# Kernel optimization log

Hardware: AMD Instinct MI355X
Metric: run time of the kernel (lower is better)

## Reference

```python
import jax, jax.numpy as jnp
import numpy as np

B, T, D, H, W = 4, 4096, 1024, 16, 64  # batch, seq, dim, heads, window_size
HD = D // H
NW = T // W  # num_windows (T divisible by W -> pad=0)


def setup_inputs() -> dict:
    key = jax.random.key(0)
    ks = jax.random.split(key, 7)
    x = jax.random.normal(ks[0], (B, T, D), dtype=jnp.float32)
    W_qkv = jax.random.normal(ks[1], (3 * D, D), dtype=jnp.float32) * 0.02
    W_out = jax.random.normal(ks[2], (D, D), dtype=jnp.float32) * 0.02
    b_out = jnp.zeros((D,), dtype=jnp.float32)
    W_cross = jax.random.normal(ks[3], (D, D), dtype=jnp.float32) * 0.02
    b_cross = jnp.zeros((D,), dtype=jnp.float32)
    jitter = jax.random.permutation(ks[4], NW)  # fixed permutation (stands in for torch.randperm)
    return {"x": x, "W_qkv": W_qkv, "W_out": W_out, "b_out": b_out,
            "W_cross": W_cross, "b_cross": b_cross, "jitter": jitter}


def reference(x, W_qkv, W_out, b_out, W_cross, b_cross, jitter):
    scale = HD ** -0.5
    # qkv projection (no bias)
    qkv = x @ W_qkv.T                      # (B,T,3D)
    q, k, v = jnp.split(qkv, 3, axis=-1)

    def to_windows(t):  # (B,T,D) -> (B,H,NW,W,HD)
        return t.reshape(B, T, H, HD).transpose(0, 2, 1, 3).reshape(B, H, NW, W, HD)

    q_w, k_w, v_w = to_windows(q), to_windows(k), to_windows(v)

    # local windowed attention
    attn = jnp.einsum('bhnqd,bhnkd->bhnqk', q_w, k_w) * scale
    attn = jax.nn.softmax(attn, axis=-1)
    local = jnp.einsum('bhnqk,bhnkd->bhnqd', attn, v_w)      # (B,H,NW,W,HD)
    local = local.reshape(B, H, T, HD).transpose(0, 2, 1, 3).reshape(B, T, D)

    # cross-window summary exchange
    scores = jnp.tanh(x @ W_cross.T + b_cross).mean(-1)       # (B,T)
    weights = jax.nn.softmax(scores.reshape(B, NW, W), axis=-1)
    summaries = jnp.einsum('bnw,bnwd->bnd', weights, x.reshape(B, NW, W, D))  # (B,NW,D)
    jittered = summaries[:, jitter, :]
    cs_attn = jax.nn.softmax(jnp.einsum('bnd,bmd->bnm', summaries, jittered) * (D ** -0.5), axis=-1)
    cs_out = jnp.einsum('bnm,bmd->bnd', cs_attn, jittered)    # (B,NW,D)
    cs_exp = jnp.broadcast_to(cs_out[:, :, None, :], (B, NW, W, D)).reshape(B, T, D)

    final = local + 0.25 * cs_exp
    return final @ W_out.T + b_out
```

## Files before the change

kernel.cpp:

```cpp
#include <hip/hip_runtime.h>

typedef unsigned short u16;
typedef float f32x4 __attribute__((ext_vector_type(4)));
typedef __bf16 bf16x8 __attribute__((ext_vector_type(8)));

#define T_ 4096
#define D_ 1024
#define NW_ 64

__device__ __forceinline__ float b2f(u16 u) {
  return __uint_as_float(((unsigned)u) << 16);
}
__device__ __forceinline__ u16 f2bf(float f) {
  unsigned u = __float_as_uint(f);
  u += 0x7fffu + ((u >> 16) & 1u);
  return (u16)(u >> 16);
}
__device__ __forceinline__ void g2l16(const u16* g, u16* l) {
  __builtin_amdgcn_global_load_lds((const __attribute__((address_space(1))) void*)g,
                                   (__attribute__((address_space(3))) void*)l, 16, 0, 0);
}

__global__ __launch_bounds__(256) void cvt3_k(const float* __restrict__ s0, u16* __restrict__ d0,
                                              const float* __restrict__ s1, u16* __restrict__ d1,
                                              const float* __restrict__ s2, u16* __restrict__ d2)
{
  long bid = blockIdx.x;
  const float* src; u16* dst; long base;
  if (bid < 16384)      { src = s0; dst = d0; base = bid * 1024; }
  else if (bid < 19456) { src = s1; dst = d1; base = (bid - 16384) * 1024; }
  else                  { src = s2; dst = d2; base = (bid - 19456) * 1024; }
  long i = base + (long)threadIdx.x * 4;
  float4 v = *(const float4*)(src + i);
  ushort4 o;
  o.x = f2bf(v.x); o.y = f2bf(v.y); o.z = f2bf(v.z); o.w = f2bf(v.w);
  *(ushort4*)(dst + i) = o;
}

__global__ __launch_bounds__(256) void cvt_k(const float* __restrict__ src,
                                             u16* __restrict__ dst, long n)
{
  long i = ((long)blockIdx.x * 256 + threadIdx.x) * 4;
  if (i >= n) return;
  float4 v = *(const float4*)(src + i);
  ushort4 o;
  o.x = f2bf(v.x); o.y = f2bf(v.y); o.z = f2bf(v.z); o.w = f2bf(v.w);
  *(ushort4*)(dst + i) = o;
}

__global__ __launch_bounds__(512, 2) void gemm256(
    const u16* __restrict__ A, const u16* __restrict__ Bm,
    u16* __restrict__ C16, float* __restrict__ C32,
    const float* __restrict__ bias, int M, int N, int K, int lda)
{
  __shared__ u16 SH[65536];
  (void)M;
  const int tid = threadIdx.x;
  const int lane = tid & 63;
  const int w = tid >> 6;
  const int wm = w >> 2, wn = w & 3;
  const int q = lane >> 4, il = lane & 15;

  const int nbx = gridDim.x;
  const int nwg = nbx * (int)gridDim.y;
  const int bid = (int)blockIdx.y * nbx + (int)blockIdx.x;
  const int nid = (bid & 7) * (nwg >> 3) + (bid >> 3);
  const long m0 = (long)(nid / nbx) * 256;
  const long n0 = (long)(nid % nbx) * 256;

  const int nt = K >> 6;
  const int ntm1 = nt - 1;

  const int u0 = tid, u1 = 512 + tid;
  const int r0 = u0 >> 3, r1 = u1 >> 3;
  const int sx0 = ((u0 & 7) ^ (r0 & 7)) << 3;
  const int sx1 = ((u1 & 7) ^ (r1 & 7)) << 3;
  const long gar0 = m0 + (r0 >> 6) * 128 + (r0 & 63);
  const long gar1 = m0 + (r1 >> 6) * 128 + (r1 & 63);
  const long gbr0 = n0 + (r0 >> 5) * 64 + (r0 & 31);
  const long gbr1 = n0 + (r1 >> 5) * 64 + (r1 & 31);
  const int dl = w * 512;

  const int aro = (wm * 64 + il) * 64;
  const int bro = (wn * 32 + il) * 64;
  const int ax = (il & 7) << 3;
  const int ko0 = (q * 8) ^ ax;
  const int ko1 = (32 + q * 8) ^ ax;

  f32x4 acc[8][4] = {};
  bf16x8 af[4][2], bf0[2][2], bf1[2][2];

#define ASP(BUF, MH) (&SH[((BUF) * 2 + (MH)) * 8192])
#define BSP(BUF, NH) (&SH[32768 + ((BUF) * 2 + (NH)) * 8192])
#define STGA(BUF, MH, KT) do { \
    g2l16(A + (gar0 + (MH) * 64) * (long)lda + (KT) * 64 + sx0, ASP(BUF, MH) + dl); \
    g2l16(A + (gar1 + (MH) * 64) * (long)lda + (KT) * 64 + sx1, ASP(BUF, MH) + 4096 + dl); \
  } while (0)
#define STGB(BUF, NH, KT) do { \
    g2l16(Bm + (gbr0 + (NH) * 32) * (long)K + (KT) * 64 + sx0, BSP(BUF, NH) + dl); \
    g2l16(Bm + (gbr1 + (NH) * 32) * (long)K + (KT) * 64 + sx1, BSP(BUF, NH) + 4096 + dl); \
  } while (0)
#define LDAF(BUF, MH) do { \
    _Pragma("unroll") for (int f = 0; f < 4; ++f) { \
      af[f][0] = *(const bf16x8*)(ASP(BUF, MH) + aro + f * 1024 + ko0); \
      af[f][1] = *(const bf16x8*)(ASP(BUF, MH) + aro + f * 1024 + ko1); \
    } } while (0)
#define LDBF(BUF, NH, BF) do { \
    _Pragma("unroll") for (int j = 0; j < 2; ++j) { \
      BF[j][0] = *(const bf16x8*)(BSP(BUF, NH) + bro + j * 1024 + ko0); \
      BF[j][1] = *(const bf16x8*)(BSP(BUF, NH) + bro + j * 1024 + ko1); \
    } } while (0)
#define MFMAQ(MH, NH, BF) do { \
    _Pragma("unroll") for (int f = 0; f < 4; ++f) { \
      _Pragma("unroll") for (int j = 0; j < 2; ++j) { \
        acc[(MH)*4+f][(NH)*2+j] = __builtin_amdgcn_mfma_f32_16x16x32_bf16(af[f][0], BF[j][0], acc[(MH)*4+f][(NH)*2+j], 0, 0, 0); \
        acc[(MH)*4+f][(NH)*2+j] = __builtin_amdgcn_mfma_f32_16x16x32_bf16(af[f][1], BF[j][1], acc[(MH)*4+f][(NH)*2+j], 0, 0, 0); \
      } } } while (0)
#define BARR() __builtin_amdgcn_s_barrier()
#define WL0() asm volatile("s_waitcnt lgkmcnt(0)" ::: "memory")
#define WV6() asm volatile("s_waitcnt vmcnt(6)" ::: "memory")
#define PRIO(x) __builtin_amdgcn_s_setprio(x)

  STGA(0, 0, 0); STGB(0, 0, 0); STGB(0, 1, 0); STGA(0, 1, 0);
  STGA(1, 0, 1); STGB(1, 0, 1); STGB(1, 1, 1);
  WV6();
  BARR();

  for (int tt = 0; tt < nt; tt += 2) {
    const int t1 = tt + 1;
    const int t2 = tt + 2 <= ntm1 ? tt + 2 : ntm1;
    const int t3 = tt + 3 <= ntm1 ? tt + 3 : ntm1;
    LDAF(0, 0); LDBF(0, 0, bf0);
    STGA(1, 1, t1);
    BARR(); WL0();
    PRIO(1); MFMAQ(0, 0, bf0); PRIO(0);
    BARR();
    LDBF(0, 1, bf1);
    STGA(0, 0, t2);
    BARR(); WL0();
    PRIO(1); MFMAQ(0, 1, bf1); PRIO(0);
    BARR();
    LDAF(0, 1);
    STGB(0, 0, t2);
    BARR(); WL0();
    PRIO(1); MFMAQ(1, 0, bf0); PRIO(0);
    BARR();
    STGB(0, 1, t2);
    BARR();
    PRIO(1); MFMAQ(1, 1, bf1); PRIO(0);
    WV6(); BARR();
    LDAF(1, 0); LDBF(1, 0, bf0);
    STGA(0, 1, t2);
    BARR(); WL0();
    PRIO(1); MFMAQ(0, 0, bf0); PRIO(0);
    BARR();
    LDBF(1, 1, bf1);
    STGA(1, 0, t3);
    BARR(); WL0();
    PRIO(1); MFMAQ(0, 1, bf1); PRIO(0);
    BARR();
    LDAF(1, 1);
    STGB(1, 0, t3);
    BARR(); WL0();
    PRIO(1); MFMAQ(1, 0, bf0); PRIO(0);
    BARR();
    STGB(1, 1, t3);
    BARR();
    PRIO(1); MFMAQ(1, 1, bf1); PRIO(0);
    WV6(); BARR();
  }

  asm volatile("s_waitcnt vmcnt(0)" ::: "memory");
  __syncthreads();

  if (C32) {
    float* Cf = (float*)SH;
#pragma unroll
    for (int h = 0; h < 2; ++h) {
      if (wm == h) {
#pragma unroll
        for (int ni = 0; ni < 4; ++ni) {
          const int ccol = wn * 64 + ni * 16 + il;
          const float bv = bias ? bias[n0 + ccol] : 0.0f;
#pragma unroll
          for (int mi = 0; mi < 8; ++mi) {
#pragma unroll
            for (int r = 0; r < 4; ++r) {
              const int crow = (mi >> 2) * 64 + (mi & 3) * 16 + q * 4 + r;
              const int byte = (crow * 1024 + ccol * 4) ^ (((crow >> 2) & 1) << 6);
              *(float*)((char*)Cf + byte) = acc[mi][ni][r] + bv;
            }
          }
        }
      }
      __syncthreads();
#pragma unroll
      for (int i = 0; i < 16; ++i) {
        const int u = i * 512 + tid;
        const int crow = u >> 6, c16 = u & 63;
        const int byte = (crow * 1024 + c16 * 16) ^ (((crow >> 2) & 1) << 6);
        float4 v = *(const float4*)((char*)Cf + byte);
        *(float4*)(C32 + (m0 + h * 128 + crow) * N + n0 + c16 * 4) = v;
      }
      __syncthreads();
    }
  } else {
    u16* Cs = (u16*)SH;
#pragma unroll
    for (int ni = 0; ni < 4; ++ni) {
      const int ccol = wn * 64 + ni * 16 + il;
      const float bv = bias ? bias[n0 + ccol] : 0.0f;
#pragma unroll
      for (int mi = 0; mi < 8; ++mi) {
#pragma unroll
        for (int r = 0; r < 4; ++r) {
          const int crow = wm * 128 + (mi >> 2) * 64 + (mi & 3) * 16 + q * 4 + r;
          const int byte = (crow * 512 + ccol * 2) ^ (((crow >> 2) & 3) << 5);
          *(u16*)((char*)Cs + byte) = f2bf(acc[mi][ni][r] + bv);
        }
      }
    }
    __syncthreads();
#pragma unroll
    for (int i = 0; i < 16; ++i) {
      const int u = i * 512 + tid;
      const int crow = u >> 5, c16 = u & 31;
      const int byte = (crow * 512 + c16 * 16) ^ (((crow >> 2) & 3) << 5);
      uint4 v = *(const uint4*)((char*)Cs + byte);
      *(uint4*)(C16 + (m0 + crow) * N + n0 + c16 * 8) = v;
    }
  }
#undef ASP
#undef BSP
#undef STGA
#undef STGB
#undef LDAF
#undef LDBF
#undef MFMAQ
#undef BARR
#undef WL0
#undef WV6
#undef PRIO
}

__global__ __launch_bounds__(256) void scores_k(const u16* __restrict__ y,
                                                float* __restrict__ scores)
{
  const int lane = threadIdx.x & 63;
  const long r = (long)blockIdx.x * 4 + (threadIdx.x >> 6);
  const u16* p = y + r * D_ + lane * 16;
  uint4 v0 = *(const uint4*)p;
  uint4 v1 = *(const uint4*)(p + 8);
  union { uint4 v; u16 s[8]; } a, c;
  a.v = v0; c.v = v1;
  float s = 0.f;
#pragma unroll
  for (int e = 0; e < 8; ++e) s += tanhf(b2f(a.s[e]));
#pragma unroll
  for (int e = 0; e < 8; ++e) s += tanhf(b2f(c.s[e]));
#pragma unroll
  for (int o = 32; o; o >>= 1) s += __shfl_xor(s, o, 64);
  if (lane == 0) scores[r] = s * (1.0f / 1024.0f);
}

__global__ __launch_bounds__(256) void summar_k(const float* __restrict__ x,
                                                const float* __restrict__ scores,
                                                float* __restrict__ summ)
{
  __shared__ float wts[64];
  const int tid = threadIdx.x;
  const int b = blockIdx.x >> 6, n = blockIdx.x & 63;
  if (tid < 64) {
    float v = scores[(long)b * T_ + n * 64 + tid];
    float mx = v;
#pragma unroll
    for (int o = 32; o; o >>= 1) mx = fmaxf(mx, __shfl_xor(mx, o, 64));
    float e = __expf(v - mx);
    float s = e;
#pragma unroll
    for (int o = 32; o; o >>= 1) s += __shfl_xor(s, o, 64);
    wts[tid] = e / s;
  }
  __syncthreads();
  const int d0 = tid * 4;
  const float* xp = x + ((long)b * T_ + n * 64) * D_ + d0;
  float a0 = 0, a1 = 0, a2 = 0, a3 = 0;
#pragma unroll 4
  for (int wd = 0; wd < 64; ++wd) {
    float4 v = *(const float4*)(xp + (long)wd * D_);
    float wv = wts[wd];
    a0 += wv * v.x; a1 += wv * v.y; a2 += wv * v.z; a3 += wv * v.w;
  }
  *(float4*)(summ + ((long)b * NW_ + n) * D_ + d0) = make_float4(a0, a1, a2, a3);
}

__global__ __launch_bounds__(256) void cross_k(const float* __restrict__ summ,
                                               const int* __restrict__ jitter,
                                               float* __restrict__ cso)
{
  __shared__ float sm[64], pm[64];
  __shared__ int jidx[64];
  const int tid = threadIdx.x;
  const int b = blockIdx.x >> 6, n = blockIdx.x & 63;
  if (tid < 64) jidx[tid] = jitter[tid];
  __syncthreads();
  const int m = tid >> 2, part = tid & 3;
  const float* sn = summ + ((long)b * NW_ + n) * D_;
  const float* sj = summ + ((long)b * NW_ + jidx[m]) * D_;
  float p = 0.f;
  for (int d = part * 256; d < part * 256 + 256; d += 4) {
    float4 aa = *(const float4*)(sn + d);
    float4 bb = *(const float4*)(sj + d);
    p += aa.x * bb.x + aa.y * bb.y + aa.z * bb.z + aa.w * bb.w;
  }
  p += __shfl_xor(p, 1, 64);
  p += __shfl_xor(p, 2, 64);
  if (part == 0) sm[m] = p * (1.0f / 32.0f);
  __syncthreads();
  if (tid < 64) {
    float v = sm[tid], mx = v;
#pragma unroll
    for (int o = 32; o; o >>= 1) mx = fmaxf(mx, __shfl_xor(mx, o, 64));
    float e = __expf(v - mx), s = e;
#pragma unroll
    for (int o = 32; o; o >>= 1) s += __shfl_xor(s, o, 64);
    pm[tid] = e / s;
  }
  __syncthreads();
  const int d0 = tid * 4;
  float a0 = 0, a1 = 0, a2 = 0, a3 = 0;
  for (int mm = 0; mm < 64; ++mm) {
    const float* sr = summ + ((long)b * NW_ + jidx[mm]) * D_ + d0;
    float wv = pm[mm];
    float4 vv = *(const float4*)sr;
    a0 += wv * vv.x; a1 += wv * vv.y; a2 += wv * vv.z; a3 += wv * vv.w;
  }
  *(float4*)(cso + ((long)b * NW_ + n) * D_ + d0) = make_float4(a0, a1, a2, a3);
}

__global__ __launch_bounds__(256) void attn_win(u16* qkv,
                                                const float* __restrict__ cso)
{
  __shared__ u16 Qs[64 * 72], Ks[64 * 72], Vt[64 * 72], Ps[64 * 72];
  unsigned* Vt32 = (unsigned*)Vt;
  const int tid = threadIdx.x;
  const int lane = tid & 63;
  const int w = tid >> 6;
  const int q = lane >> 4, il = lane & 15;
  const int bid = blockIdx.x;
  const int n = bid & 63;
  const int h = (bid >> 6) & 15;
  const int b = bid >> 10;
  const long rowbase = (long)b * T_ + n * 64;

#pragma unroll
  for (int i = 0; i < 2; ++i) {
    int u = i * 256 + tid;
    int row = u >> 3, cp = u & 7;
    const u16* src = qkv + (rowbase + row) * 3072 + h * 64 + cp * 8;
    uint4 qv = *(const uint4*)src;
    uint4 kv = *(const uint4*)(src + 1024);
    uint4 vv = *(const uint4*)(src + 2048);
    *(uint4*)&Qs[row * 72 + cp * 8] = qv;
    *(uint4*)&Ks[row * 72 + cp * 8] = kv;
    union { uint4 v; unsigned u[4]; } mine, part;
    mine.v = vv;
#pragma unroll
    for (int m = 0; m < 4; ++m) part.u[m] = __shfl_xor(mine.u[m], 8, 64);
    const bool even = ((row & 1) == 0);
    const int p = row >> 1;
#pragma unroll
    for (int m = 0; m < 4; ++m) {
      unsigned word = even ? ((mine.u[m] & 0xffffu) | (part.u[m] << 16))
                           : ((part.u[m] >> 16)     | (mine.u[m] & 0xffff0000u));
      int c = cp * 8 + 2 * m + (even ? 0 : 1);
      Vt32[c * 36 + p] = word;
    }
  }
  __syncthreads();

  f32x4 sacc[4] = {};
#pragma unroll
  for (int ks = 0; ks < 2; ++ks) {
    bf16x8 aq = *(const bf16x8*)&Qs[(w * 16 + il) * 72 + ks * 32 + q * 8];
#pragma unroll
    for (int ct = 0; ct < 4; ++ct) {
      bf16x8 bk = *(const bf16x8*)&Ks[(ct * 16 + il) * 72 + ks * 32 + q * 8];
      sacc[ct] = __builtin_amdgcn_mfma_f32_16x16x32_bf16(aq, bk, sacc[ct], 0, 0, 0);
    }
  }

#pragma unroll
  for (int r = 0; r < 4; ++r) {
    float s0 = sacc[0][r] * 0.125f, s1 = sacc[1][r] * 0.125f,
          s2 = sacc[2][r] * 0.125f, s3 = sacc[3][r] * 0.125f;
    float mx = fmaxf(fmaxf(s0, s1), fmaxf(s2, s3));
#pragma unroll
    for (int o = 1; o < 16; o <<= 1) mx = fmaxf(mx, __shfl_xor(mx, o, 64));
    float e0 = __expf(s0 - mx), e1 = __expf(s1 - mx),
          e2 = __expf(s2 - mx), e3 = __expf(s3 - mx);
    float sum = e0 + e1 + e2 + e3;
#pragma unroll
    for (int o = 1; o < 16; o <<= 1) sum += __shfl_xor(sum, o, 64);
    float inv = 1.0f / sum;
    int prow = w * 16 + q * 4 + r;
    Ps[prow * 72 + 0 * 16 + il] = f2bf(e0 * inv);
    Ps[prow * 72 + 1 * 16 + il] = f2bf(e1 * inv);
    Ps[prow * 72 + 2 * 16 + il] = f2bf(e2 * inv);
    Ps[prow * 72 + 3 * 16 + il] = f2bf(e3 * inv);
  }
  __syncthreads();

  f32x4 oacc[4] = {};
#pragma unroll
  for (int ks = 0; ks < 2; ++ks) {
    bf16x8 ap = *(const bf16x8*)&Ps[(w * 16 + il) * 72 + ks * 32 + q * 8];
#pragma unroll
    for (int dt = 0; dt < 4; ++dt) {
      bf16x8 bv = *(const bf16x8*)&Vt[(dt * 16 + il) * 72 + ks * 32 + q * 8];
      oacc[dt] = __builtin_amdgcn_mfma_f32_16x16x32_bf16(ap, bv, oacc[dt], 0, 0, 0);
    }
  }

  const float* cs = cso + ((long)b * NW_ + n) * D_ + h * 64;
#pragma unroll
  for (int dt = 0; dt < 4; ++dt) {
    int col = dt * 16 + il;
    float cadd = 0.25f * cs[col];
#pragma unroll
    for (int r = 0; r < 4; ++r) {
      int row = w * 16 + q * 4 + r;
      qkv[(rowbase + row) * 3072 + h * 64 + col] = f2bf(oacc[dt][r] + cadd);
    }
  }
}

extern "C" void kernel_launch(void* const* d_in, const int* in_sizes, int n_in,
                              void* d_out, int out_size, void* d_ws, size_t ws_size,
                              hipStream_t stream)
{
  (void)in_sizes; (void)n_in; (void)out_size; (void)ws_size;
  const float* x      = (const float*)d_in[0];
  const float* Wqkv   = (const float*)d_in[1];
  const float* Wout   = (const float*)d_in[2];
  const float* bout   = (const float*)d_in[3];
  const float* Wcross = (const float*)d_in[4];
  const float* bcross = (const float*)d_in[5];
  const int*   jitter = (const int*)d_in[6];
  float* out = (float*)d_out;

  char* ws = (char*)d_ws;
  u16*   qkv    = (u16*)ws;
  u16*   y      = (u16*)ws;
  u16*   xb     = (u16*)(ws + 100663296);
  u16*   wqkvb  = (u16*)(ws + 134217728);
  u16*   wtmp   = (u16*)(ws + 140509184);
  float* scores = (float*)(ws + 142606336);
  float* summ   = (float*)(ws + 142671872);
  float* cso    = (float*)(ws + 143720448);

  dim3 blk(256);
  dim3 gblk(512);
  cvt3_k<<<20480, blk, 0, stream>>>(x, xb, Wqkv, wqkvb, Wcross, wtmp);
  gemm256<<<dim3(4, 64), gblk, 0, stream>>>(xb, wtmp, y, nullptr, bcross, 16384, 1024, 1024, 1024);
  cvt_k<<<1024, blk, 0, stream>>>(Wout, wtmp, 1048576L);
  scores_k<<<4096, blk, 0, stream>>>(y, scores);
  summar_k<<<256, blk, 0, stream>>>(x, scores, summ);
  cross_k<<<256, blk, 0, stream>>>(summ, jitter, cso);
  gemm256<<<dim3(12, 64), gblk, 0, stream>>>(xb, wqkvb, qkv, nullptr, nullptr, 16384, 3072, 1024, 1024);
  attn_win<<<4096, blk, 0, stream>>>(qkv, cso);
  gemm256<<<dim3(4, 64), gblk, 0, stream>>>(qkv, wtmp, nullptr, out, bout, 16384, 1024, 1024, 3072);
}
```

Baseline: 379.0 us.

## Software-pipeline LDS fragment loads with MFMA using double-buffered A registers

Restructures the GEMM main loop so the LDS fragment reads for the next quarter-tile are issued before the MFMA block of the current one. This uses a second A-fragment register set and drops the explicit lgkmcnt(0) waits. The global-to-LDS staging wait changes from vmcnt(6) to vmcnt(8), and one barrier per quarter is removed. The aim is to hide LDS latency and cut barrier stalls, at the cost of more VGPRs and a riskier ordering of LDS reuse against in-flight staging writes.

```diff
diff --git a/kernel.cpp b/kernel.cpp
--- a/kernel.cpp
+++ b/kernel.cpp
@@ -88,7 +88,7 @@
   const int ko1 = (32 + q * 8) ^ ax;
 
   f32x4 acc[8][4] = {};
-  bf16x8 af[4][2], bf0[2][2], bf1[2][2];
+  bf16x8 afA[4][2], afB[4][2], bf0[2][2], bf1[2][2];
 
 #define ASP(BUF, MH) (&SH[((BUF) * 2 + (MH)) * 8192])
 #define BSP(BUF, NH) (&SH[32768 + ((BUF) * 2 + (NH)) * 8192])
@@ -100,74 +100,66 @@
     g2l16(Bm + (gbr0 + (NH) * 32) * (long)K + (KT) * 64 + sx0, BSP(BUF, NH) + dl); \
     g2l16(Bm + (gbr1 + (NH) * 32) * (long)K + (KT) * 64 + sx1, BSP(BUF, NH) + 4096 + dl); \
   } while (0)
-#define LDAF(BUF, MH) do { \
+#define LDAF(BUF, MH, AF) do { \
     _Pragma("unroll") for (int f = 0; f < 4; ++f) { \
-      af[f][0] = *(const bf16x8*)(ASP(BUF, MH) + aro + f * 1024 + ko0); \
-      af[f][1] = *(const bf16x8*)(ASP(BUF, MH) + aro + f * 1024 + ko1); \
+      AF[f][0] = *(const bf16x8*)(ASP(BUF, MH) + aro + f * 1024 + ko0); \
+      AF[f][1] = *(const bf16x8*)(ASP(BUF, MH) + aro + f * 1024 + ko1); \
     } } while (0)
 #define LDBF(BUF, NH, BF) do { \
     _Pragma("unroll") for (int j = 0; j < 2; ++j) { \
       BF[j][0] = *(const bf16x8*)(BSP(BUF, NH) + bro + j * 1024 + ko0); \
       BF[j][1] = *(const bf16x8*)(BSP(BUF, NH) + bro + j * 1024 + ko1); \
     } } while (0)
-#define MFMAQ(MH, NH, BF) do { \
+#define MFMAQ(MH, NH, AF, BF) do { \
     _Pragma("unroll") for (int f = 0; f < 4; ++f) { \
       _Pragma("unroll") for (int j = 0; j < 2; ++j) { \
-        acc[(MH)*4+f][(NH)*2+j] = __builtin_amdgcn_mfma_f32_16x16x32_bf16(af[f][0], BF[j][0], acc[(MH)*4+f][(NH)*2+j], 0, 0, 0); \
-        acc[(MH)*4+f][(NH)*2+j] = __builtin_amdgcn_mfma_f32_16x16x32_bf16(af[f][1], BF[j][1], acc[(MH)*4+f][(NH)*2+j], 0, 0, 0); \
+        acc[(MH)*4+f][(NH)*2+j] = __builtin_amdgcn_mfma_f32_16x16x32_bf16(AF[f][0], BF[j][0], acc[(MH)*4+f][(NH)*2+j], 0, 0, 0); \
+        acc[(MH)*4+f][(NH)*2+j] = __builtin_amdgcn_mfma_f32_16x16x32_bf16(AF[f][1], BF[j][1], acc[(MH)*4+f][(NH)*2+j], 0, 0, 0); \
       } } } while (0)
 #define BARR() __builtin_amdgcn_s_barrier()
-#define WL0() asm volatile("s_waitcnt lgkmcnt(0)" ::: "memory")
-#define WV6() asm volatile("s_waitcnt vmcnt(6)" ::: "memory")
+#define WV8() asm volatile("s_waitcnt vmcnt(8)" ::: "memory")
 #define PRIO(x) __builtin_amdgcn_s_setprio(x)
 
   STGA(0, 0, 0); STGB(0, 0, 0); STGB(0, 1, 0); STGA(0, 1, 0);
   STGA(1, 0, 1); STGB(1, 0, 1); STGB(1, 1, 1);
-  WV6();
+  WV8();
   BARR();
+  LDAF(0, 0, afA); LDBF(0, 0, bf0);
 
   for (int tt = 0; tt < nt; tt += 2) {
     const int t1 = tt + 1;
     const int t2 = tt + 2 <= ntm1 ? tt + 2 : ntm1;
     const int t3 = tt + 3 <= ntm1 ? tt + 3 : ntm1;
-    LDAF(0, 0); LDBF(0, 0, bf0);
+    LDBF(0, 1, bf1);
+    PRIO(1); MFMAQ(0, 0, afA, bf0); PRIO(0);
     STGA(1, 1, t1);
-    BARR(); WL0();
-    PRIO(1); MFMAQ(0, 0, bf0); PRIO(0);
+    WV8(); BARR();
+    LDAF(0, 1, afB);
+    PRIO(1); MFMAQ(0, 1, afA, bf1); PRIO(0);
+    STGA(0, 0, t2);
     BARR();
-    LDBF(0, 1, bf1);
-    STGA(0, 0, t2);
-    BARR(); WL0();
-    PRIO(1); MFMAQ(0, 1, bf1); PRIO(0);
+    PRIO(1); MFMAQ(1, 0, afB, bf0); PRIO(0);
+    STGB(0, 0, t2);
+    WV8(); BARR();
+    LDAF(1, 0, afA); LDBF(1, 0, bf0);
+    PRIO(1); MFMAQ(1, 1, afB, bf1); PRIO(0);
+    STGB(0, 1, t2);
+    WV8(); BARR();
+    LDBF(1, 1, bf1);
+    PRIO(1); MFMAQ(0, 0, afA, bf0); PRIO(0);
+    STGA(0, 1, t2);
+    WV8(); BARR();
+    LDAF(1, 1, afB);
+    PRIO(1); MFMAQ(0, 1, afA, bf1); PRIO(0);
+    STGA(1, 0, t3);
     BARR();
-    LDAF(0, 1);
-    STGB(0, 0, t2);
-    BARR(); WL0();
-    PRIO(1); MFMAQ(1, 0, bf0); PRIO(0);
-    BARR();
-    STGB(0, 1, t2);
-    BARR();
-    PRIO(1); MFMAQ(1, 1, bf1); PRIO(0);
-    WV6(); BARR();
-    LDAF(1, 0); LDBF(1, 0, bf0);
-    STGA(0, 1, t2);
-    BARR(); WL0();
-    PRIO(1); MFMAQ(0, 0, bf0); PRIO(0);
-    BARR();
-    LDBF(1, 1, bf1);
-    STGA(1, 0, t3);
-    BARR(); WL0();
-    PRIO(1); MFMAQ(0, 1, bf1); PRIO(0);
-    BARR();
-    LDAF(1, 1);
+    PRIO(1); MFMAQ(1, 0, afB, bf0); PRIO(0);
     STGB(1, 0, t3);
-    BARR(); WL0();
-    PRIO(1); MFMAQ(1, 0, bf0); PRIO(0);
-    BARR();
+    WV8(); BARR();
+    LDAF(0, 0, afA); LDBF(0, 0, bf0);
+    PRIO(1); MFMAQ(1, 1, afB, bf1); PRIO(0);
     STGB(1, 1, t3);
-    BARR();
-    PRIO(1); MFMAQ(1, 1, bf1); PRIO(0);
-    WV6(); BARR();
+    WV8(); BARR();
   }
 
   asm volatile("s_waitcnt vmcnt(0)" ::: "memory");
@@ -238,8 +230,7 @@
 #undef LDBF
 #undef MFMAQ
 #undef BARR
-#undef WL0
-#undef WV6
+#undef WV8
 #undef PRIO
 }
 
```

Result: slower. 411.0 us (+8.4%).

## Fuse cross-score GEMM and tanh-mean reduction into the QKV GEMM launch

Applied to the files above, without the earlier changes.

Extends the QKV GEMM grid with four extra column blocks that multiply x by W_cross. This relies on the bf16 W_cross buffer sitting right after W_qkv in the workspace. Those blocks apply bias and tanh in registers, reduce each row across lanes and waves, and write per-tile partial scores, which summar_k sums. This drops the bf16 y intermediate write and read, the separate scores_k kernel and one GEMM launch, and gives a larger grid with better tail balance. The cost is a heavier epilogue in those blocks, reliance on the adjacent buffer layout, and reuse of d_out as scratch for the cross-summary output.

```diff
diff --git a/kernel.cpp b/kernel.cpp
--- a/kernel.cpp
+++ b/kernel.cpp
@@ -51,7 +51,8 @@
 __global__ __launch_bounds__(512, 2) void gemm256(
     const u16* __restrict__ A, const u16* __restrict__ Bm,
     u16* __restrict__ C16, float* __restrict__ C32,
-    const float* __restrict__ bias, int M, int N, int K, int lda)
+    const float* __restrict__ bias, int M, int N, int K, int lda,
+    float* __restrict__ scores4, const float* __restrict__ bias_y)
 {
   __shared__ u16 SH[65536];
   (void)M;
@@ -88,7 +89,7 @@
   const int ko1 = (32 + q * 8) ^ ax;
 
   f32x4 acc[8][4] = {};
-  bf16x8 af[4][2], bf0[2][2], bf1[2][2];
+  bf16x8 af[4], bf0[2][2], bf1[2][2];
 
 #define ASP(BUF, MH) (&SH[((BUF) * 2 + (MH)) * 8192])
 #define BSP(BUF, NH) (&SH[32768 + ((BUF) * 2 + (NH)) * 8192])
@@ -102,8 +103,8 @@
   } while (0)
 #define LDAF(BUF, MH) do { \
     _Pragma("unroll") for (int f = 0; f < 4; ++f) { \
-      af[f][0] = *(const bf16x8*)(ASP(BUF, MH) + aro + f * 1024 + ko0); \
-      af[f][1] = *(const bf16x8*)(ASP(BUF, MH) + aro + f * 1024 + ko1); \
+      af[f] = *(const bf16x8*)(ASP(BUF, MH) + aro + f * 1024 + ko0); \
+      afk[f] = *(const bf16x8*)(ASP(BUF, MH) + aro + f * 1024 + ko1); \
     } } while (0)
 #define LDBF(BUF, NH, BF) do { \
     _Pragma("unroll") for (int j = 0; j < 2; ++j) { \
@@ -113,13 +114,15 @@
 #define MFMAQ(MH, NH, BF) do { \
     _Pragma("unroll") for (int f = 0; f < 4; ++f) { \
       _Pragma("unroll") for (int j = 0; j < 2; ++j) { \
-        acc[(MH)*4+f][(NH)*2+j] = __builtin_amdgcn_mfma_f32_16x16x32_bf16(af[f][0], BF[j][0], acc[(MH)*4+f][(NH)*2+j], 0, 0, 0); \
-        acc[(MH)*4+f][(NH)*2+j] = __builtin_amdgcn_mfma_f32_16x16x32_bf16(af[f][1], BF[j][1], acc[(MH)*4+f][(NH)*2+j], 0, 0, 0); \
+        acc[(MH)*4+f][(NH)*2+j] = __builtin_amdgcn_mfma_f32_16x16x32_bf16(af[f], BF[j][0], acc[(MH)*4+f][(NH)*2+j], 0, 0, 0); \
+        acc[(MH)*4+f][(NH)*2+j] = __builtin_amdgcn_mfma_f32_16x16x32_bf16(afk[f], BF[j][1], acc[(MH)*4+f][(NH)*2+j], 0, 0, 0); \
       } } } while (0)
 #define BARR() __builtin_amdgcn_s_barrier()
 #define WL0() asm volatile("s_waitcnt lgkmcnt(0)" ::: "memory")
 #define WV6() asm volatile("s_waitcnt vmcnt(6)" ::: "memory")
 #define PRIO(x) __builtin_amdgcn_s_setprio(x)
+
+  bf16x8 afk[4];
 
   STGA(0, 0, 0); STGB(0, 0, 0); STGB(0, 1, 0); STGA(0, 1, 0);
   STGA(1, 0, 1); STGB(1, 0, 1); STGB(1, 1, 1);
@@ -172,6 +175,35 @@
 
   asm volatile("s_waitcnt vmcnt(0)" ::: "memory");
   __syncthreads();
+
+  if (scores4 && n0 >= N) {
+    float* part = (float*)SH;
+    const int sub = (int)((n0 - N) >> 8);
+    float bv[4];
+#pragma unroll
+    for (int ni = 0; ni < 4; ++ni)
+      bv[ni] = bias_y ? bias_y[(n0 - N) + wn * 64 + ni * 16 + il] : 0.0f;
+#pragma unroll
+    for (int mi = 0; mi < 8; ++mi) {
+#pragma unroll
+      for (int r = 0; r < 4; ++r) {
+        float s = tanhf(acc[mi][0][r] + bv[0]) + tanhf(acc[mi][1][r] + bv[1])
+                + tanhf(acc[mi][2][r] + bv[2]) + tanhf(acc[mi][3][r] + bv[3]);
+#pragma unroll
+        for (int o = 1; o < 16; o <<= 1) s += __shfl_xor(s, o, 64);
+        if (il == 0) {
+          const int rowl = wm * 128 + (mi >> 2) * 64 + (mi & 3) * 16 + q * 4 + r;
+          part[rowl * 4 + wn] = s;
+        }
+      }
+    }
+    __syncthreads();
+    if (tid < 256) {
+      float t = part[tid * 4] + part[tid * 4 + 1] + part[tid * 4 + 2] + part[tid * 4 + 3];
+      scores4[(m0 + tid) * 4 + sub] = t;
+    }
+    return;
+  }
 
   if (C32) {
     float* Cf = (float*)SH;
@@ -243,35 +275,16 @@
 #undef PRIO
 }
 
-__global__ __launch_bounds__(256) void scores_k(const u16* __restrict__ y,
-                                                float* __restrict__ scores)
-{
-  const int lane = threadIdx.x & 63;
-  const long r = (long)blockIdx.x * 4 + (threadIdx.x >> 6);
-  const u16* p = y + r * D_ + lane * 16;
-  uint4 v0 = *(const uint4*)p;
-  uint4 v1 = *(const uint4*)(p + 8);
-  union { uint4 v; u16 s[8]; } a, c;
-  a.v = v0; c.v = v1;
-  float s = 0.f;
-#pragma unroll
-  for (int e = 0; e < 8; ++e) s += tanhf(b2f(a.s[e]));
-#pragma unroll
-  for (int e = 0; e < 8; ++e) s += tanhf(b2f(c.s[e]));
-#pragma unroll
-  for (int o = 32; o; o >>= 1) s += __shfl_xor(s, o, 64);
-  if (lane == 0) scores[r] = s * (1.0f / 1024.0f);
-}
-
 __global__ __launch_bounds__(256) void summar_k(const float* __restrict__ x,
-                                                const float* __restrict__ scores,
+                                                const float* __restrict__ s4,
                                                 float* __restrict__ summ)
 {
   __shared__ float wts[64];
   const int tid = threadIdx.x;
   const int b = blockIdx.x >> 6, n = blockIdx.x & 63;
   if (tid < 64) {
-    float v = scores[(long)b * T_ + n * 64 + tid];
+    const long r4 = ((long)b * T_ + n * 64 + tid) * 4;
+    float v = (s4[r4] + s4[r4 + 1] + s4[r4 + 2] + s4[r4 + 3]) * (1.0f / 1024.0f);
     float mx = v;
 #pragma unroll
     for (int o = 32; o; o >>= 1) mx = fmaxf(mx, __shfl_xor(mx, o, 64));
@@ -450,24 +463,23 @@
   float* out = (float*)d_out;
 
   char* ws = (char*)d_ws;
-  u16*   qkv    = (u16*)ws;
-  u16*   y      = (u16*)ws;
-  u16*   xb     = (u16*)(ws + 100663296);
-  u16*   wqkvb  = (u16*)(ws + 134217728);
-  u16*   wtmp   = (u16*)(ws + 140509184);
-  float* scores = (float*)(ws + 142606336);
-  float* summ   = (float*)(ws + 142671872);
-  float* cso    = (float*)(ws + 143720448);
+  u16*   qkv     = (u16*)ws;
+  u16*   xb      = (u16*)(ws + 100663296);
+  u16*   wqkvb   = (u16*)(ws + 134217728);
+  u16*   wtmp    = (u16*)(ws + 140509184);
+  float* scores4 = (float*)(ws + 142606336);
+  float* summ    = (float*)(ws + 142868480);
+  float* cso     = (float*)d_out;
 
   dim3 blk(256);
   dim3 gblk(512);
   cvt3_k<<<20480, blk, 0, stream>>>(x, xb, Wqkv, wqkvb, Wcross, wtmp);
-  gemm256<<<dim3(4, 64), gblk, 0, stream>>>(xb, wtmp, y, nullptr, bcross, 16384, 1024, 1024, 1024);
+  gemm256<<<dim3(16, 64), gblk, 0, stream>>>(xb, wqkvb, qkv, nullptr, nullptr,
+                                             16384, 3072, 1024, 1024, scores4, bcross);
   cvt_k<<<1024, blk, 0, stream>>>(Wout, wtmp, 1048576L);
-  scores_k<<<4096, blk, 0, stream>>>(y, scores);
-  summar_k<<<256, blk, 0, stream>>>(x, scores, summ);
+  summar_k<<<256, blk, 0, stream>>>(x, scores4, summ);
   cross_k<<<256, blk, 0, stream>>>(summ, jitter, cso);
-  gemm256<<<dim3(12, 64), gblk, 0, stream>>>(xb, wqkvb, qkv, nullptr, nullptr, 16384, 3072, 1024, 1024);
   attn_win<<<4096, blk, 0, stream>>>(qkv, cso);
-  gemm256<<<dim3(4, 64), gblk, 0, stream>>>(qkv, wtmp, nullptr, out, bout, 16384, 1024, 1024, 3072);
-}
+  gemm256<<<dim3(4, 64), gblk, 0, stream>>>(qkv, wtmp, nullptr, out, bout,
+                                            16384, 1024, 1024, 3072, nullptr, nullptr);
+}
```

New measurement: 394.2 us. +4.0%, slower.
